# Optimization experiments

Measured on AMD Instinct MI355X. Metric: run time of the kernel, lower is better.

## Reference

```python
import jax, jax.numpy as jnp
import numpy as np

N_NODES = 50000
N_EDGES = 800000
EMB = 100
LAYERS = 3
EPS = 1e-12  # torch F.normalize default eps


def setup_inputs() -> dict:
    key = jax.random.key(0)
    k1, k2, k3, k4 = jax.random.split(key, 4)
    adj_row = jax.random.randint(k1, (N_EDGES,), 0, N_NODES, dtype=jnp.int32)
    adj_col = jax.random.randint(k2, (N_EDGES,), 0, N_NODES, dtype=jnp.int32)
    adj_val = jax.random.uniform(k3, (N_EDGES,), dtype=jnp.float32)
    embedding = jax.random.normal(k4, (N_NODES, EMB), dtype=jnp.float32)
    a = jnp.ones((LAYERS + 1, 1, 1), dtype=jnp.float32)  # init.ones_
    return {"adj_row": adj_row, "adj_col": adj_col, "adj_val": adj_val,
            "embedding": embedding, "a": a}


def reference(adj_row, adj_col, adj_val, embedding, a):
    def spmm(x):
        # sparse.mm(A, x): gather source rows, scale by edge value, scatter-add to dest rows
        return jax.ops.segment_sum(adj_val[:, None] * x[adj_col], adj_row,
                                   num_segments=N_NODES)

    outs = [embedding]
    x = embedding
    for _ in range(LAYERS):
        x = spmm(x)
        outs.append(x)
    final = jnp.stack(outs, axis=0)  # [L+1, N, d]
    # F.normalize(..., dim=-1, p=2): x / max(||x||_2, eps)
    norm = jnp.sqrt(jnp.sum(final * final, axis=-1, keepdims=True))
    final = final / jnp.maximum(norm, EPS)
    return jnp.sum(a * final, axis=0)  # [N, d]
```

## Files before the change

kernel.cpp:

```cpp
#include <hip/hip_runtime.h>
#include <hip/hip_bf16.h>

#define N_NODES 50000
#define N_EDGES 800000
#define EMB 100
#define HALF_EMB 50
#define ROW_U4 16
#define ROW_B2 64
#define NORM_EPS 1e-12f
#define BROWS 128
#define NB ((N_NODES + BROWS - 1) / BROWS)
#define CAP 4096
#define EPB 16384
#define SCAT_BLOCKS ((N_EDGES + EPB - 1) / EPB)
#define CONV_BLOCKS 3125

#define SEL_LO 0x01000504u
#define SEL_HI 0x03020706u

__global__ __launch_bounds__(1024) void scatter_conv(
        const int* __restrict__ adj_row, const int* __restrict__ adj_col,
        const float* __restrict__ adj_val, int* __restrict__ bucket_cnt,
        int2* __restrict__ slab,
        const float* __restrict__ emb, float* __restrict__ norm0,
        __hip_bfloat162* __restrict__ xb) {
    const int t = threadIdx.x;
    if (blockIdx.x >= SCAT_BLOCKS) {
        int wave = (blockIdx.x - SCAT_BLOCKS) * 16 + (t >> 6);
        int lane = t & 63;
        if (wave >= N_NODES) return;
        float2 v = make_float2(0.0f, 0.0f);
        if (lane < HALF_EMB) v = ((const float2*)emb)[(size_t)wave * HALF_EMB + lane];
        float s = v.x * v.x + v.y * v.y;
        #pragma unroll
        for (int off = 32; off > 0; off >>= 1) s += __shfl_xor(s, off);
        if (lane == 0) norm0[wave] = sqrtf(s);
        __hip_bfloat162 b;
        b.x = __float2bfloat16(v.x);
        b.y = __float2bfloat16(v.y);
        xb[(size_t)wave * ROW_B2 + lane] = b;
        return;
    }
    __shared__ int hist[NB];
    __shared__ int cur[NB];
    const int base_e = blockIdx.x * EPB;
    for (int i = t; i < NB; i += 1024) hist[i] = 0;
    __syncthreads();
    int rows[EPB / 1024];
    #pragma unroll
    for (int j = 0; j < EPB / 1024; ++j) {
        int e = base_e + j * 1024 + t;
        int r = (e < N_EDGES) ? adj_row[e] : -1;
        rows[j] = r;
        if (r >= 0) atomicAdd(&hist[r >> 7], 1);
    }
    __syncthreads();
    for (int i = t; i < NB; i += 1024) {
        int c = hist[i];
        cur[i] = (c > 0) ? atomicAdd(&bucket_cnt[i], c) : 0;
    }
    __syncthreads();
    #pragma unroll
    for (int j = 0; j < EPB / 1024; ++j) {
        int e = base_e + j * 1024 + t;
        int r = rows[j];
        if (r >= 0) {
            int b = r >> 7;
            int p = atomicAdd(&cur[b], 1);
            unsigned rc = ((unsigned)r << 16) | (unsigned)adj_col[e];
            slab[(size_t)b * CAP + p] = make_int2((int)rc, __float_as_int(adj_val[e]));
        }
    }
}

__global__ __launch_bounds__(1024) void csr_build(
        const int* __restrict__ bucket_cnt, const int2* __restrict__ slab,
        unsigned* __restrict__ csr4, int* __restrict__ row_ptr) {
    __shared__ int hist[BROWS];
    __shared__ int wsum[16];
    __shared__ int wtot[2];
    __shared__ int base_sh;
    const int b = blockIdx.x, t = threadIdx.x;
    const int lane = t & 63, wid = t >> 6;
    int pv = (t < b) ? bucket_cnt[t] : 0;
    #pragma unroll
    for (int off = 32; off > 0; off >>= 1) pv += __shfl_xor(pv, off);
    if (lane == 0) wsum[wid] = pv;
    if (t < BROWS) hist[t] = 0;
    const int cnt = bucket_cnt[b];
    __syncthreads();
    if (t == 0) {
        int s_ = 0;
        #pragma unroll
        for (int i = 0; i < 16; ++i) s_ += wsum[i];
        base_sh = s_;
    }
    for (int i = t; i < cnt; i += 1024)
        atomicAdd(&hist[(int)(((unsigned)slab[(size_t)b * CAP + i].x) >> 16) & (BROWS - 1)], 1);
    __syncthreads();
    const int base = base_sh;
    int v = (t < BROWS) ? hist[t] : 0;
    int sc = v;
    #pragma unroll
    for (int off = 1; off < 64; off <<= 1) {
        int n = __shfl_up(sc, off);
        if (lane >= off) sc += n;
    }
    if (t < BROWS && lane == 63) wtot[wid] = sc;
    __syncthreads();
    if (wid == 1 && t < BROWS) sc += wtot[0];
    int ex = sc - v;
    if (t < BROWS) {
        hist[t] = ex;
        int gr = b * BROWS + t;
        if (gr < N_NODES) row_ptr[gr] = base + ex;
    }
    if (b == 0 && t == 0) row_ptr[N_NODES] = N_EDGES;
    __syncthreads();
    for (int i = t; i < cnt; i += 1024) {
        int2 e = slab[(size_t)b * CAP + i];
        int l = (int)(((unsigned)e.x) >> 16) & (BROWS - 1);
        int p = atomicAdd(&hist[l], 1);
        unsigned col = (unsigned)e.x & 0xFFFFu;
        __hip_bfloat16 hv = __float2bfloat16(__int_as_float(e.y));
        unsigned vb = (unsigned)*reinterpret_cast<unsigned short*>(&hv);
        csr4[base + p] = (col << 16) | vb;
    }
}

__device__ inline float dot2b(unsigned a, unsigned b, float c) {
    float d;
    asm("v_dot2_f32_bf16 %0, %1, %2, %3" : "=v"(d) : "v"(a), "v"(b), "v"(c));
    return d;
}

__device__ inline void dot8pair(unsigned ra, unsigned rb, uint4 ua, uint4 ub,
                                float4& accL, float4& accH) {
    unsigned vp = __builtin_amdgcn_perm(ra, rb, SEL_LO);
    accL.x = dot2b(vp, __builtin_amdgcn_perm(ua.x, ub.x, SEL_LO), accL.x);
    accL.y = dot2b(vp, __builtin_amdgcn_perm(ua.x, ub.x, SEL_HI), accL.y);
    accL.z = dot2b(vp, __builtin_amdgcn_perm(ua.y, ub.y, SEL_LO), accL.z);
    accL.w = dot2b(vp, __builtin_amdgcn_perm(ua.y, ub.y, SEL_HI), accL.w);
    accH.x = dot2b(vp, __builtin_amdgcn_perm(ua.z, ub.z, SEL_LO), accH.x);
    accH.y = dot2b(vp, __builtin_amdgcn_perm(ua.z, ub.z, SEL_HI), accH.y);
    accH.z = dot2b(vp, __builtin_amdgcn_perm(ua.w, ub.w, SEL_LO), accH.z);
    accH.w = dot2b(vp, __builtin_amdgcn_perm(ua.w, ub.w, SEL_HI), accH.w);
}

__device__ inline void up8(uint4 u, float4& lo, float4& hi) {
    lo.x = __uint_as_float(u.x << 16);
    lo.y = __uint_as_float(u.x & 0xFFFF0000u);
    lo.z = __uint_as_float(u.y << 16);
    lo.w = __uint_as_float(u.y & 0xFFFF0000u);
    hi.x = __uint_as_float(u.z << 16);
    hi.y = __uint_as_float(u.z & 0xFFFF0000u);
    hi.z = __uint_as_float(u.w << 16);
    hi.w = __uint_as_float(u.w & 0xFFFF0000u);
}

__device__ inline unsigned pack2(float a, float b) {
    __hip_bfloat16 x = __float2bfloat16(a), y = __float2bfloat16(b);
    return (unsigned)*(unsigned short*)&x | ((unsigned)*(unsigned short*)&y << 16);
}

__global__ void spmm_fused(const int* __restrict__ row_ptr,
                           const unsigned* __restrict__ csr4,
                           const uint4* __restrict__ xb,
                           uint4* __restrict__ yb,
                           float* __restrict__ norm_out,
                           const float* __restrict__ a,
                           const uint4* __restrict__ ep0,
                           const uint4* __restrict__ ep1,
                           const float* __restrict__ norms,
                           float* __restrict__ out,
                           int final_layer) {
    int wave = blockIdx.x * (blockDim.x >> 6) + (threadIdx.x >> 6);
    int lane = threadIdx.x & 63;
    if (wave >= N_NODES) return;
    int start = row_ptr[wave];
    int end   = row_ptr[wave + 1];
    int deg   = end - start;
    unsigned myrec = (lane < deg) ? csr4[start + lane] : 0u;
    int g = lane >> 4, c = lane & 15;
    float4 accL = make_float4(0.0f, 0.0f, 0.0f, 0.0f);
    float4 accH = make_float4(0.0f, 0.0f, 0.0f, 0.0f);
    int dn  = (deg < 64) ? deg : 64;
    int dn4 = (dn + 3) & ~3;
    int d = 0;
    for (; d + 16 <= dn4; d += 16) {
        unsigned ra = __shfl(myrec, d + g);
        unsigned rb = __shfl(myrec, d + 4 + g);
        unsigned rc = __shfl(myrec, d + 8 + g);
        unsigned rd = __shfl(myrec, d + 12 + g);
        uint4 ua = xb[(size_t)(ra >> 16) * ROW_U4 + c];
        uint4 ub = xb[(size_t)(rb >> 16) * ROW_U4 + c];
        uint4 uc = xb[(size_t)(rc >> 16) * ROW_U4 + c];
        uint4 ud = xb[(size_t)(rd >> 16) * ROW_U4 + c];
        dot8pair(ra, rb, ua, ub, accL, accH);
        dot8pair(rc, rd, uc, ud, accL, accH);
    }
    for (; d + 8 <= dn4; d += 8) {
        unsigned ra = __shfl(myrec, d + g);
        unsigned rb = __shfl(myrec, d + 4 + g);
        uint4 ua = xb[(size_t)(ra >> 16) * ROW_U4 + c];
        uint4 ub = xb[(size_t)(rb >> 16) * ROW_U4 + c];
        dot8pair(ra, rb, ua, ub, accL, accH);
    }
    for (; d < dn4; d += 4) {
        unsigned r = __shfl(myrec, d + g);
        uint4 u = xb[(size_t)(r >> 16) * ROW_U4 + c];
        float v = __uint_as_float(r << 16);
        float4 l, h;
        up8(u, l, h);
        accL.x += v * l.x; accL.y += v * l.y; accL.z += v * l.z; accL.w += v * l.w;
        accH.x += v * h.x; accH.y += v * h.y; accH.z += v * h.z; accH.w += v * h.w;
    }
    for (int e = start + 64; e < end; e += 4) {
        unsigned r = (e + g < end) ? csr4[e + g] : 0u;
        uint4 u = xb[(size_t)(r >> 16) * ROW_U4 + c];
        float v = __uint_as_float(r << 16);
        float4 l, h;
        up8(u, l, h);
        accL.x += v * l.x; accL.y += v * l.y; accL.z += v * l.z; accL.w += v * l.w;
        accH.x += v * h.x; accH.y += v * h.y; accH.z += v * h.z; accH.w += v * h.w;
    }
    accL.x += __shfl_xor(accL.x, 16); accL.x += __shfl_xor(accL.x, 32);
    accL.y += __shfl_xor(accL.y, 16); accL.y += __shfl_xor(accL.y, 32);
    accL.z += __shfl_xor(accL.z, 16); accL.z += __shfl_xor(accL.z, 32);
    accL.w += __shfl_xor(accL.w, 16); accL.w += __shfl_xor(accL.w, 32);
    accH.x += __shfl_xor(accH.x, 16); accH.x += __shfl_xor(accH.x, 32);
    accH.y += __shfl_xor(accH.y, 16); accH.y += __shfl_xor(accH.y, 32);
    accH.z += __shfl_xor(accH.z, 16); accH.z += __shfl_xor(accH.z, 32);
    accH.w += __shfl_xor(accH.w, 16); accH.w += __shfl_xor(accH.w, 32);
    float s = accL.x * accL.x + accL.y * accL.y + accL.z * accL.z + accL.w * accL.w
            + accH.x * accH.x + accH.y * accH.y + accH.z * accH.z + accH.w * accH.w;
    s += __shfl_xor(s, 1); s += __shfl_xor(s, 2);
    s += __shfl_xor(s, 4); s += __shfl_xor(s, 8);
    if (!final_layer) {
        if (g == 0) {
            uint4 o;
            o.x = pack2(accL.x, accL.y);
            o.y = pack2(accL.z, accL.w);
            o.z = pack2(accH.x, accH.y);
            o.w = pack2(accH.z, accH.w);
            yb[(size_t)wave * ROW_U4 + c] = o;
        }
        if (lane == 0) norm_out[wave] = sqrtf(s);
    } else {
        float s0 = a[0] / fmaxf(norms[wave], NORM_EPS);
        float s1 = a[1] / fmaxf(norms[N_NODES + wave], NORM_EPS);
        float s2 = a[2] / fmaxf(norms[2 * N_NODES + wave], NORM_EPS);
        float s3 = a[3] / fmaxf(sqrtf(s), NORM_EPS);
        if (g == 0 && c < 13) {
            size_t idx = (size_t)wave * ROW_U4 + c;
            float4 f0l, f0h, f1l, f1h, f2l, f2h;
            up8(ep0[idx], f0l, f0h);
            up8(ep1[idx], f1l, f1h);
            up8(xb[idx],  f2l, f2h);
            float4 o0, o1;
            o0.x = s0 * f0l.x + s1 * f1l.x + s2 * f2l.x + s3 * accL.x;
            o0.y = s0 * f0l.y + s1 * f1l.y + s2 * f2l.y + s3 * accL.y;
            o0.z = s0 * f0l.z + s1 * f1l.z + s2 * f2l.z + s3 * accL.z;
            o0.w = s0 * f0l.w + s1 * f1l.w + s2 * f2l.w + s3 * accL.w;
            o1.x = s0 * f0h.x + s1 * f1h.x + s2 * f2h.x + s3 * accH.x;
            o1.y = s0 * f0h.y + s1 * f1h.y + s2 * f2h.y + s3 * accH.y;
            o1.z = s0 * f0h.z + s1 * f1h.z + s2 * f2h.z + s3 * accH.z;
            o1.w = s0 * f0h.w + s1 * f1h.w + s2 * f2h.w + s3 * accH.w;
            float4* out4 = (float4*)out;
            size_t fb = (size_t)wave * 25;
            if (c < 12) {
                out4[fb + 2 * c]     = o0;
                out4[fb + 2 * c + 1] = o1;
            } else {
                out4[fb + 24] = o0;
            }
        }
    }
}

extern "C" void kernel_launch(void* const* d_in, const int* in_sizes, int n_in,
                              void* d_out, int out_size, void* d_ws, size_t ws_size,
                              hipStream_t stream) {
    const int*   adj_row   = (const int*)d_in[0];
    const int*   adj_col   = (const int*)d_in[1];
    const float* adj_val   = (const float*)d_in[2];
    const float* embedding = (const float*)d_in[3];
    const float* a         = (const float*)d_in[4];
    float* out = (float*)d_out;

    int2* slab     = (int2*)d_ws;
    unsigned* csr4 = (unsigned*)(slab + (size_t)NB * CAP);
    uint4* xbE = (uint4*)(csr4 + N_EDGES);
    uint4* xb1 = xbE + (size_t)N_NODES * ROW_U4;
    float* norms = (float*)(xb1 + (size_t)N_NODES * ROW_U4);
    int* row_ptr    = (int*)(norms + 3 * N_NODES);
    int* bucket_cnt = row_ptr + (N_NODES + 1);
    uint4* xb2 = (uint4*)slab;

    const int node_blocks = (N_NODES + 3) / 4;

    hipMemsetAsync(bucket_cnt, 0, sizeof(int) * NB, stream);
    scatter_conv<<<SCAT_BLOCKS + CONV_BLOCKS, 1024, 0, stream>>>(
        adj_row, adj_col, adj_val, bucket_cnt, slab,
        embedding, norms, (__hip_bfloat162*)xbE);
    csr_build<<<NB, 1024, 0, stream>>>(bucket_cnt, slab, csr4, row_ptr);

    spmm_fused<<<node_blocks, 256, 0, stream>>>(row_ptr, csr4, xbE,
                                                xb1, norms + N_NODES, a,
                                                nullptr, nullptr, nullptr,
                                                nullptr, 0);
    spmm_fused<<<node_blocks, 256, 0, stream>>>(row_ptr, csr4, xb1,
                                                xb2, norms + 2 * N_NODES, a,
                                                nullptr, nullptr, nullptr,
                                                nullptr, 0);
    spmm_fused<<<node_blocks, 256, 0, stream>>>(row_ptr, csr4, xb2,
                                                nullptr, nullptr, a,
                                                xbE, xb1, norms,
                                                out, 1);
}
```

Measured before the change: 216.4 us.

## Replace bucket-slab CSR build with degree histogram, scan, and atomic scatter

Changes how the CSR is built. The old scheme scattered edges into per-bucket slabs and then sorted each bucket in shared memory. The new one counts per-row degrees with global atomics, scans them into row_ptr and a cursor array, and then scatters each edge straight into csr4 with an atomic on its row cursor. This drops the intermediate slab write and re-read, but adds 800K global atomics in each of two passes, adds a kernel launch, and makes the order of edges within a row nondeterministic.

```diff
diff --git a/kernel.cpp b/kernel.cpp
--- a/kernel.cpp
+++ b/kernel.cpp
@@ -10,23 +10,22 @@
 #define NORM_EPS 1e-12f
 #define BROWS 128
 #define NB ((N_NODES + BROWS - 1) / BROWS)
-#define CAP 4096
-#define EPB 16384
-#define SCAT_BLOCKS ((N_EDGES + EPB - 1) / EPB)
+#define HB 98
+#define EPB_H 8192
 #define CONV_BLOCKS 3125
+#define SCAT_BLOCKS ((N_EDGES + 1023) / 1024)
 
 #define SEL_LO 0x01000504u
 #define SEL_HI 0x03020706u
 
-__global__ __launch_bounds__(1024) void scatter_conv(
-        const int* __restrict__ adj_row, const int* __restrict__ adj_col,
-        const float* __restrict__ adj_val, int* __restrict__ bucket_cnt,
-        int2* __restrict__ slab,
+__global__ __launch_bounds__(1024) void hist_conv(
+        const int* __restrict__ adj_row, int* __restrict__ deg,
+        int* __restrict__ bucket_cnt,
         const float* __restrict__ emb, float* __restrict__ norm0,
         __hip_bfloat162* __restrict__ xb) {
     const int t = threadIdx.x;
-    if (blockIdx.x >= SCAT_BLOCKS) {
-        int wave = (blockIdx.x - SCAT_BLOCKS) * 16 + (t >> 6);
+    if (blockIdx.x >= HB) {
+        int wave = (blockIdx.x - HB) * 16 + (t >> 6);
         int lane = t & 63;
         if (wave >= N_NODES) return;
         float2 v = make_float2(0.0f, 0.0f);
@@ -41,42 +40,29 @@
         xb[(size_t)wave * ROW_B2 + lane] = b;
         return;
     }
-    __shared__ int hist[NB];
-    __shared__ int cur[NB];
-    const int base_e = blockIdx.x * EPB;
-    for (int i = t; i < NB; i += 1024) hist[i] = 0;
+    __shared__ int bh[NB];
+    for (int i = t; i < NB; i += 1024) bh[i] = 0;
     __syncthreads();
-    int rows[EPB / 1024];
+    const int base_e = blockIdx.x * EPB_H;
     #pragma unroll
-    for (int j = 0; j < EPB / 1024; ++j) {
+    for (int j = 0; j < EPB_H / 1024; ++j) {
         int e = base_e + j * 1024 + t;
-        int r = (e < N_EDGES) ? adj_row[e] : -1;
-        rows[j] = r;
-        if (r >= 0) atomicAdd(&hist[r >> 7], 1);
+        if (e < N_EDGES) {
+            int r = adj_row[e];
+            atomicAdd(&deg[r], 1);
+            atomicAdd(&bh[r >> 7], 1);
+        }
     }
     __syncthreads();
     for (int i = t; i < NB; i += 1024) {
-        int c = hist[i];
-        cur[i] = (c > 0) ? atomicAdd(&bucket_cnt[i], c) : 0;
-    }
-    __syncthreads();
-    #pragma unroll
-    for (int j = 0; j < EPB / 1024; ++j) {
-        int e = base_e + j * 1024 + t;
-        int r = rows[j];
-        if (r >= 0) {
-            int b = r >> 7;
-            int p = atomicAdd(&cur[b], 1);
-            unsigned rc = ((unsigned)r << 16) | (unsigned)adj_col[e];
-            slab[(size_t)b * CAP + p] = make_int2((int)rc, __float_as_int(adj_val[e]));
-        }
-    }
-}
-
-__global__ __launch_bounds__(1024) void csr_build(
-        const int* __restrict__ bucket_cnt, const int2* __restrict__ slab,
-        unsigned* __restrict__ csr4, int* __restrict__ row_ptr) {
-    __shared__ int hist[BROWS];
+        int c = bh[i];
+        if (c > 0) atomicAdd(&bucket_cnt[i], c);
+    }
+}
+
+__global__ __launch_bounds__(1024) void scan_rowptr(
+        const int* __restrict__ bucket_cnt, const int* __restrict__ deg,
+        int* __restrict__ row_ptr, int* __restrict__ cursor) {
     __shared__ int wsum[16];
     __shared__ int wtot[2];
     __shared__ int base_sh;
@@ -86,8 +72,6 @@
     #pragma unroll
     for (int off = 32; off > 0; off >>= 1) pv += __shfl_xor(pv, off);
     if (lane == 0) wsum[wid] = pv;
-    if (t < BROWS) hist[t] = 0;
-    const int cnt = bucket_cnt[b];
     __syncthreads();
     if (t == 0) {
         int s_ = 0;
@@ -95,11 +79,8 @@
         for (int i = 0; i < 16; ++i) s_ += wsum[i];
         base_sh = s_;
     }
-    for (int i = t; i < cnt; i += 1024)
-        atomicAdd(&hist[(int)(((unsigned)slab[(size_t)b * CAP + i].x) >> 16) & (BROWS - 1)], 1);
-    __syncthreads();
-    const int base = base_sh;
-    int v = (t < BROWS) ? hist[t] : 0;
+    const int gr = b * BROWS + t;
+    int v = (t < BROWS && gr < N_NODES) ? deg[gr] : 0;
     int sc = v;
     #pragma unroll
     for (int off = 1; off < 64; off <<= 1) {
@@ -108,24 +89,27 @@
     }
     if (t < BROWS && lane == 63) wtot[wid] = sc;
     __syncthreads();
+    const int base = base_sh;
     if (wid == 1 && t < BROWS) sc += wtot[0];
     int ex = sc - v;
-    if (t < BROWS) {
-        hist[t] = ex;
-        int gr = b * BROWS + t;
-        if (gr < N_NODES) row_ptr[gr] = base + ex;
+    if (t < BROWS && gr < N_NODES) {
+        row_ptr[gr] = base + ex;
+        cursor[gr]  = base + ex;
     }
     if (b == 0 && t == 0) row_ptr[N_NODES] = N_EDGES;
-    __syncthreads();
-    for (int i = t; i < cnt; i += 1024) {
-        int2 e = slab[(size_t)b * CAP + i];
-        int l = (int)(((unsigned)e.x) >> 16) & (BROWS - 1);
-        int p = atomicAdd(&hist[l], 1);
-        unsigned col = (unsigned)e.x & 0xFFFFu;
-        __hip_bfloat16 hv = __float2bfloat16(__int_as_float(e.y));
-        unsigned vb = (unsigned)*reinterpret_cast<unsigned short*>(&hv);
-        csr4[base + p] = (col << 16) | vb;
-    }
+}
+
+__global__ __launch_bounds__(1024) void csr_scatter(
+        const int* __restrict__ adj_row, const int* __restrict__ adj_col,
+        const float* __restrict__ adj_val,
+        int* __restrict__ cursor, unsigned* __restrict__ csr4) {
+    int e = blockIdx.x * 1024 + threadIdx.x;
+    if (e >= N_EDGES) return;
+    int r = adj_row[e];
+    int p = atomicAdd(&cursor[r], 1);
+    __hip_bfloat16 hv = __float2bfloat16(adj_val[e]);
+    unsigned vb = (unsigned)*reinterpret_cast<unsigned short*>(&hv);
+    csr4[p] = ((unsigned)adj_col[e] << 16) | vb;
 }
 
 __device__ inline float dot2b(unsigned a, unsigned b, float c) {
@@ -288,22 +272,24 @@
     const float* a         = (const float*)d_in[4];
     float* out = (float*)d_out;
 
-    int2* slab     = (int2*)d_ws;
-    unsigned* csr4 = (unsigned*)(slab + (size_t)NB * CAP);
+    unsigned* csr4 = (unsigned*)d_ws;
     uint4* xbE = (uint4*)(csr4 + N_EDGES);
     uint4* xb1 = xbE + (size_t)N_NODES * ROW_U4;
-    float* norms = (float*)(xb1 + (size_t)N_NODES * ROW_U4);
+    uint4* xb2 = xb1 + (size_t)N_NODES * ROW_U4;
+    float* norms = (float*)(xb2 + (size_t)N_NODES * ROW_U4);
     int* row_ptr    = (int*)(norms + 3 * N_NODES);
-    int* bucket_cnt = row_ptr + (N_NODES + 1);
-    uint4* xb2 = (uint4*)slab;
+    int* deg        = row_ptr + (N_NODES + 1);
+    int* bucket_cnt = deg + N_NODES;
+    int* cursor     = bucket_cnt + NB;
 
     const int node_blocks = (N_NODES + 3) / 4;
 
-    hipMemsetAsync(bucket_cnt, 0, sizeof(int) * NB, stream);
-    scatter_conv<<<SCAT_BLOCKS + CONV_BLOCKS, 1024, 0, stream>>>(
-        adj_row, adj_col, adj_val, bucket_cnt, slab,
-        embedding, norms, (__hip_bfloat162*)xbE);
-    csr_build<<<NB, 1024, 0, stream>>>(bucket_cnt, slab, csr4, row_ptr);
+    hipMemsetAsync(deg, 0, sizeof(int) * (N_NODES + NB), stream);
+    hist_conv<<<HB + CONV_BLOCKS, 1024, 0, stream>>>(
+        adj_row, deg, bucket_cnt, embedding, norms, (__hip_bfloat162*)xbE);
+    scan_rowptr<<<NB, 1024, 0, stream>>>(bucket_cnt, deg, row_ptr, cursor);
+    csr_scatter<<<SCAT_BLOCKS, 1024, 0, stream>>>(
+        adj_row, adj_col, adj_val, cursor, csr4);
 
     spmm_fused<<<node_blocks, 256, 0, stream>>>(row_ptr, csr4, xbE,
                                                 xb1, norms + N_NODES, a,
```

After: 267.0 us. 1.23x slower.
